# Kernel optimization log

Hardware: AMD Instinct MI355X
Metric: run time of the kernel (lower is better)

The kernel has to match this reference:

```python
import jax, jax.numpy as jnp
import numpy as np

HIDDEN = 512
HEAD = 64
SEQ = 2048
CHUNK = 256
GAMMA = 0.96875
SCALE_BASE = 512.0


def _xpos(x, downscale):
    # x: [B, L, hd]; XPOS with offset=0 (scale rows == length, no trimming needed)
    B, L, hd = x.shape
    half = hd // 2
    scale_vec = (jnp.arange(0, hd, 2, dtype=jnp.float32) + 0.4 * hd) / (1.4 * hd)  # [half]
    power = jnp.arange(L, dtype=jnp.float32) / SCALE_BASE                          # [L]
    scale = scale_vec[None, :] ** power[:, None]                                   # [L, half]
    inv_freq = 1.0 / (10000.0 ** (jnp.arange(half, dtype=jnp.float32) / half))
    sinusoid = jnp.arange(L, dtype=jnp.float32)[:, None] * inv_freq[None, :]       # [L, half]
    sin, cos = jnp.sin(sinusoid), jnp.cos(sinusoid)
    if downscale:
        scale = 1.0 / scale
    # duplicate_interleave: repeat each column twice -> [L, hd]
    sin_f = jnp.repeat(sin * scale, 2, axis=-1)
    cos_f = jnp.repeat(cos * scale, 2, axis=-1)
    x1 = x[:, :, 0::2]
    x2 = x[:, :, 1::2]
    rot = jnp.stack((-x2, x1), axis=-1).reshape(B, L, hd)  # rotate_every_two
    return x * cos_f + rot * sin_f


def _D_parallel():
    # D[i, j] = gamma^|i-j| if j < (i//chunk + 1)*chunk else 0 (block-causal with in-chunk lookahead)
    i = jnp.arange(SEQ)[:, None]
    j = jnp.arange(SEQ)[None, :]
    j_max = (i // CHUNK + 1) * CHUNK
    decay = GAMMA ** jnp.abs(i - j).astype(jnp.float32)
    return jnp.where(j < j_max, decay, 0.0)  # gamma>0 so no NaNs to scrub


def setup_inputs() -> dict:
    key = jax.random.key(0)
    k1, k2, k3, k4 = jax.random.split(key, 4)
    X = jax.random.normal(k1, (8, SEQ, HIDDEN), dtype=jnp.float32)
    W_Q = jax.random.normal(k2, (HIDDEN, HEAD), dtype=jnp.float32) / HIDDEN
    W_K = jax.random.normal(k3, (HIDDEN, HEAD), dtype=jnp.float32) / HIDDEN
    W_V = jax.random.normal(k4, (HIDDEN, HEAD), dtype=jnp.float32) / HIDDEN
    return {"X": X, "W_Q": W_Q, "W_K": W_K, "W_V": W_V}


def reference(X, W_Q, W_K, W_V):
    Q = _xpos(X @ W_Q, downscale=False)   # [B, S, H]
    K = _xpos(X @ W_K, downscale=True)    # [B, S, H]
    V = X @ W_V                           # [B, S, V]
    D = _D_parallel()                     # [S, S]
    scores = jnp.einsum('bqh,bkh->bqk', Q, K) * D[None]
    return jnp.einsum('bqk,bkv->bqv', scores, V)
```

## Files before the change

kernel.cpp:

```cpp
#include <hip/hip_runtime.h>
#include <hip/hip_bf16.h>


typedef __attribute__((ext_vector_type(8))) short short8;
typedef __attribute__((ext_vector_type(4))) float floatx4;

#define LOG2GAMMA (-0.04580350f)
#define GINV      (1.0f / 0.96875f)

static __device__ __forceinline__ unsigned short f2bf(float f) {
    __hip_bfloat16 h = __float2bfloat16(f);
    return *reinterpret_cast<unsigned short*>(&h);
}


__global__ __launch_bounds__(256) void prep_kernel(
    const float* __restrict__ Wq, const float* __restrict__ Wk,
    const float* __restrict__ Wv,
    __hip_bfloat16* __restrict__ Wfrag, float* __restrict__ tabs)
{
    int idx = blockIdx.x * 256 + threadIdx.x;
    const int WF_N = 192 * 512;
    if (idx < WF_N) {
        int j    = idx & 7;
        int n15  = (idx >> 3) & 15;
        int quad = (idx >> 7) & 3;
        int kkg  = (idx >> 9) & 15;
        int tile = idx >> 13;
        int n = tile * 16 + n15;
        int k = kkg * 32 + quad * 8 + j;
        int m = n >> 6, c = n & 63;
        const float* W = (m == 0) ? Wq : ((m == 1) ? Wk : Wv);
        Wfrag[idx] = __float2bfloat16(W[k * 64 + c]);
    } else {
        int t2 = idx - WF_N;
        if (t2 < 4 * 2048 * 32) {
            int tab = t2 >> 16;
            int rem = t2 & 65535;
            int pos = rem >> 5;
            int t   = rem & 31;
            float inv_freq = powf(10000.0f, -(float)t / 32.0f);
            float sinus = (float)pos * inv_freq;
            float s = sinf(sinus), c = cosf(sinus);
            float sv = (2.0f * (float)t + 0.4f * 64.0f) / (1.4f * 64.0f);
            float power = (float)pos / 512.0f;
            float scl = powf(sv, (tab >= 2) ? -power : power);
            tabs[t2] = ((tab & 1) == 0) ? c * scl : s * scl;
        }
    }
}

__global__ __launch_bounds__(256, 4) void proj_kernel(
    const float* __restrict__ X, const __hip_bfloat16* __restrict__ Wfrag,
    const float* __restrict__ tabs,
    __hip_bfloat16* __restrict__ Qfrag, __hip_bfloat16* __restrict__ Kfrag,
    __hip_bfloat16* __restrict__ Vfrag, __hip_bfloat16* __restrict__ Ktfrag)
{
    __shared__ __hip_bfloat16 smem[32 * 520];

    int tid = threadIdx.x;
    int r0 = blockIdx.x * 32;
    int nh = tid >> 6, lane = tid & 63, quad = lane >> 4, l15 = lane & 15;

#pragma unroll
    for (int u = 0; u < 16; u++) {
        int f = u * 256 + tid;
        int row = f >> 7, c = f & 127;
        float4 v = *(const float4*)(X + (r0 + row) * 512 + c * 4);
        ushort4 pk;
        pk.x = f2bf(v.x); pk.y = f2bf(v.y); pk.z = f2bf(v.z); pk.w = f2bf(v.w);
        *(ushort4*)&smem[row * 520 + c * 4] = pk;
    }
    __syncthreads();

    floatx4 acc[6];
#pragma unroll
    for (int t = 0; t < 6; t++) acc[t] = (floatx4){0.f, 0.f, 0.f, 0.f};

#pragma unroll
    for (int ks = 0; ks < 16; ks++) {
        short8 a0 = *(const short8*)&smem[l15 * 520 + ks * 32 + quad * 8];
        short8 a1 = *(const short8*)&smem[(16 + l15) * 520 + ks * 32 + quad * 8];
#pragma unroll
        for (int tl = 0; tl < 3; tl++) {
            int tile = nh * 3 + tl;
            short8 bfr = *(const short8*)(Wfrag + ((tile * 16 + ks) * 64 + lane) * 8);
            acc[tl * 2 + 0] = __builtin_amdgcn_mfma_f32_16x16x32_bf16(a0, bfr, acc[tl * 2 + 0], 0, 0, 0);
            acc[tl * 2 + 1] = __builtin_amdgcn_mfma_f32_16x16x32_bf16(a1, bfr, acc[tl * 2 + 1], 0, 0, 0);
        }
    }
    __syncthreads();

    __hip_bfloat16* bufQ = smem;
    __hip_bfloat16* bufK = smem + 2304;
    __hip_bfloat16* bufV = smem + 4608;
    int b = r0 >> 11, n0 = r0 & 2047;

#pragma unroll
    for (int tl = 0; tl < 3; tl++) {
        int t = nh * 3 + tl;
#pragma unroll
        for (int r = 0; r < 2; r++) {
#pragma unroll
            for (int rg = 0; rg < 4; rg++) {
                int row = r * 16 + quad * 4 + rg;
                int n = n0 + row;
                float val = acc[tl * 2 + r][rg];
                float prt = __shfl_xor(val, 1, 64);
                if (t < 4) {
                    int ch = t * 16 + l15, tt = ch >> 1;
                    float co = tabs[n * 32 + tt];
                    float si = tabs[65536 + n * 32 + tt];
                    float o = (l15 & 1) ? (val * co + prt * si) : (val * co - prt * si);
                    bufQ[row * 72 + ch] = __float2bfloat16(o);
                } else if (t < 8) {
                    int ch = (t - 4) * 16 + l15, tt = ch >> 1;
                    float co = tabs[131072 + n * 32 + tt];
                    float si = tabs[196608 + n * 32 + tt];
                    float o = (l15 & 1) ? (val * co + prt * si) : (val * co - prt * si);
                    bufK[row * 72 + ch] = __float2bfloat16(o);
                } else {
                    int ch = (t - 8) * 16 + l15;
                    bufV[ch * 40 + row] = __float2bfloat16(val);
                }
            }
        }
    }
    __syncthreads();

    {
        int tile2 = tid >> 7, kk = (tid >> 6) & 1, ln = tid & 63;
        int q2 = ln >> 4, m15 = ln & 15;
        size_t qkbase = ((((size_t)b * 128 + (n0 >> 4) + tile2) * 2 + kk) * 64 + ln) * 8;
        uint4 vq = *(const uint4*)&bufQ[(tile2 * 16 + m15) * 72 + kk * 32 + q2 * 8];
        *(uint4*)(Qfrag + qkbase) = vq;
        uint4 vk = *(const uint4*)&bufK[(tile2 * 16 + m15) * 72 + kk * 32 + q2 * 8];
        *(uint4*)(Kfrag + qkbase) = vk;
        int t2 = tid >> 6;
        uint4 vv = *(const uint4*)&bufV[(t2 * 16 + m15) * 40 + q2 * 8];
        *(uint4*)(Vfrag + ((((size_t)b * 64 + (n0 >> 5)) * 4 + t2) * 64 + ln) * 8) = vv;
    }
    {
        int wdt = tid >> 6, ln2 = tid & 63;
        int q2 = ln2 >> 4, m15 = ln2 & 15;
        int jb0 = (n0 & 255) + q2 * 8;
        float sc = exp2f(LOG2GAMMA * (float)(255 - jb0));
        short8 pk;
#pragma unroll
        for (int jj = 0; jj < 8; jj++) {
            float v = __bfloat162float(bufK[(q2 * 8 + jj) * 72 + wdt * 16 + m15]) * sc;
            pk[jj] = (short)f2bf(v);
            sc *= GINV;
        }
        int c = n0 >> 8, ksg = (n0 >> 5) & 7;
        *(short8*)(Ktfrag + ((((size_t)(b * 8 + c) * 4 + wdt) * 8 + ksg) * 64 + ln2) * 8) = pk;
    }
}

__global__ __launch_bounds__(256, 2) void zk_kernel(
    const __hip_bfloat16* __restrict__ Ktfrag,
    const __hip_bfloat16* __restrict__ Vfrag, float* __restrict__ Zf)
{
    __shared__ float zz[64 * 68];

    int tid = threadIdx.x;
    int b = blockIdx.x >> 4, c = (blockIdx.x >> 1) & 7, kh = blockIdx.x & 1;
    int w = tid >> 6, lane = tid & 63, quad = lane >> 4, l15 = lane & 15;

    floatx4 acc[4];
#pragma unroll
    for (int t = 0; t < 4; t++) acc[t] = (floatx4){0.f, 0.f, 0.f, 0.f};

#pragma unroll
    for (int ks = 0; ks < 4; ks++) {
        int ksg = kh * 4 + ks;
        short8 a = *(const short8*)(Ktfrag +
            ((((size_t)(b * 8 + c) * 4 + w) * 8 + ksg) * 64 + lane) * 8);
#pragma unroll
        for (int vt = 0; vt < 4; vt++) {
            short8 bfr = *(const short8*)(Vfrag +
                ((((size_t)b * 64 + c * 8 + ksg) * 4 + vt) * 64 + lane) * 8);
            acc[vt] = __builtin_amdgcn_mfma_f32_16x16x32_bf16(a, bfr, acc[vt], 0, 0, 0);
        }
    }
#pragma unroll
    for (int vt = 0; vt < 4; vt++)
#pragma unroll
        for (int rg = 0; rg < 4; rg++)
            zz[(w * 16 + quad * 4 + rg) * 68 + vt * 16 + l15] = acc[vt][rg];
    __syncthreads();

    {
        int vt = tid >> 6;
#pragma unroll
        for (int kk = 0; kk < 2; kk++) {
            float v[8];
#pragma unroll
            for (int jd = 0; jd < 8; jd++)
                v[jd] = zz[(kk * 32 + quad * 8 + jd) * 68 + vt * 16 + l15];
            float* zp = Zf +
                ((((((size_t)(b * 8 + c) * 2 + kh) * 4 + vt) * 2 + kk) * 64 + lane) * 8);
            *(float4*)zp       = (float4){v[0], v[1], v[2], v[3]};
            *(float4*)(zp + 4) = (float4){v[4], v[5], v[6], v[7]};
        }
    }
}

__global__ __launch_bounds__(128, 4) void attn_kernel(
    const __hip_bfloat16* __restrict__ Qfrag, const __hip_bfloat16* __restrict__ Kfrag,
    const __hip_bfloat16* __restrict__ Vfrag, const float* __restrict__ Zf,
    float* __restrict__ out)
{
    __shared__ __hip_bfloat16 P[2 * 16 * 132];
    __shared__ float obuf[16 * 68];

    int tid = threadIdx.x;
    int b = blockIdx.x >> 7, qt = blockIdx.x & 127;
    int qc = qt >> 4;
    int h = tid >> 6, lane = tid & 63, quad = lane >> 4, l15 = lane & 15;
    __hip_bfloat16* Pw = P + h * 2112;

    short8 qf[2];
#pragma unroll
    for (int kk = 0; kk < 2; kk++)
        qf[kk] = *(const short8*)(Qfrag + (((size_t)(b * 128 + qt) * 2 + kk) * 64 + lane) * 8);

    floatx4 o[4];
#pragma unroll
    for (int t = 0; t < 4; t++) o[t] = (floatx4){0.f, 0.f, 0.f, 0.f};

    int il0 = (qt & 15) * 16 + quad * 4;

#pragma unroll
    for (int g = 0; g < 2; g++) {
        floatx4 s[4];
#pragma unroll
        for (int t = 0; t < 4; t++) s[t] = (floatx4){0.f, 0.f, 0.f, 0.f};
#pragma unroll
        for (int t = 0; t < 4; t++) {
            int kt = qc * 16 + h * 8 + g * 4 + t;
#pragma unroll
            for (int kk = 0; kk < 2; kk++) {
                short8 bfr = *(const short8*)(Kfrag +
                    (((size_t)(b * 128 + kt) * 2 + kk) * 64 + lane) * 8);
                s[t] = __builtin_amdgcn_mfma_f32_16x16x32_bf16(qf[kk], bfr, s[t], 0, 0, 0);
            }
        }
#pragma unroll
        for (int t = 0; t < 4; t++) {
            int jl = h * 128 + (g * 4 + t) * 16 + l15;
#pragma unroll
            for (int rg = 0; rg < 4; rg++) {
                int d = il0 + rg - jl; d = (d < 0) ? -d : d;
                float p = s[t][rg] * exp2f(LOG2GAMMA * (float)d);
                Pw[(quad * 4 + rg) * 132 + (g * 4 + t) * 16 + l15] = __float2bfloat16(p);
            }
        }
    }
#pragma unroll
    for (int ks = 0; ks < 4; ks++) {
        short8 a = *(const short8*)&Pw[l15 * 132 + ks * 32 + quad * 8];
#pragma unroll
        for (int vt = 0; vt < 4; vt++) {
            short8 bfr = *(const short8*)(Vfrag +
                ((((size_t)b * 64 + qc * 8 + h * 4 + ks) * 4 + vt) * 64 + lane) * 8);
            o[vt] = __builtin_amdgcn_mfma_f32_16x16x32_bf16(a, bfr, o[vt], 0, 0, 0);
        }
    }

    if (qc > 0) {
        floatx4 oc[4];
#pragma unroll
        for (int t = 0; t < 4; t++) oc[t] = (floatx4){0.f, 0.f, 0.f, 0.f};
        int nz = (qc < 3) ? qc : 3;
        float cm1 = exp2f(LOG2GAMMA * 256.0f);
        float cm2 = exp2f(LOG2GAMMA * 512.0f);
#pragma unroll
        for (int vt = 0; vt < 4; vt++) {
            float hv[8];
#pragma unroll
            for (int jd = 0; jd < 8; jd++) hv[jd] = 0.f;
            for (int m = 0; m < nz; m++) {
                float cm = (m == 0) ? 1.0f : ((m == 1) ? cm1 : cm2);
#pragma unroll
                for (int kh = 0; kh < 2; kh++) {
                    const float* zp = Zf +
                        ((((((size_t)(b * 8 + qc - 1 - m) * 2 + kh) * 4 + vt) * 2 + h) * 64 + lane) * 8);
                    float4 z0 = *(const float4*)zp;
                    float4 z1 = *(const float4*)(zp + 4);
                    hv[0] += cm * z0.x; hv[1] += cm * z0.y;
                    hv[2] += cm * z0.z; hv[3] += cm * z0.w;
                    hv[4] += cm * z1.x; hv[5] += cm * z1.y;
                    hv[6] += cm * z1.z; hv[7] += cm * z1.w;
                }
            }
            short8 hb;
#pragma unroll
            for (int jd = 0; jd < 8; jd++) hb[jd] = (short)f2bf(hv[jd]);
            oc[vt] = __builtin_amdgcn_mfma_f32_16x16x32_bf16(qf[h], hb, oc[vt], 0, 0, 0);
        }
        float rs[4];
#pragma unroll
        for (int rg = 0; rg < 4; rg++)
            rs[rg] = exp2f(LOG2GAMMA * (float)(il0 + rg + 1));
#pragma unroll
        for (int vt = 0; vt < 4; vt++)
#pragma unroll
            for (int rg = 0; rg < 4; rg++)
                o[vt][rg] += oc[vt][rg] * rs[rg];
    }

    if (h == 1) {
#pragma unroll
        for (int vt = 0; vt < 4; vt++)
#pragma unroll
            for (int rg = 0; rg < 4; rg++)
                obuf[(quad * 4 + rg) * 68 + vt * 16 + l15] = o[vt][rg];
    }
    __syncthreads();
    if (h == 0) {
        int rbase = b * 2048 + qt * 16 + quad * 4;
#pragma unroll
        for (int vt = 0; vt < 4; vt++)
#pragma unroll
            for (int rg = 0; rg < 4; rg++)
                out[(size_t)(rbase + rg) * 64 + vt * 16 + l15] =
                    o[vt][rg] + obuf[(quad * 4 + rg) * 68 + vt * 16 + l15];
    }
}

extern "C" void kernel_launch(void* const* d_in, const int* in_sizes, int n_in,
                              void* d_out, int out_size, void* d_ws, size_t ws_size,
                              hipStream_t stream) {
    const float* X  = (const float*)d_in[0];
    const float* Wq = (const float*)d_in[1];
    const float* Wk = (const float*)d_in[2];
    const float* Wv = (const float*)d_in[3];
    float* out = (float*)d_out;

    char* ws = (char*)d_ws;
    __hip_bfloat16* Wfrag  = (__hip_bfloat16*)(ws);
    float*          tabs   = (float*)(ws + 196608);
    __hip_bfloat16* Qfrag  = (__hip_bfloat16*)(ws + 1245184);
    __hip_bfloat16* Kfrag  = (__hip_bfloat16*)(ws + 3342336);
    __hip_bfloat16* Vfrag  = (__hip_bfloat16*)(ws + 5439488);
    __hip_bfloat16* Ktfrag = (__hip_bfloat16*)(ws + 7536640);
    float*          Zf     = (float*)(ws + 9633792);

    prep_kernel<<<1408, 256, 0, stream>>>(Wq, Wk, Wv, Wfrag, tabs);
    proj_kernel<<<512, 256, 0, stream>>>(X, Wfrag, tabs, Qfrag, Kfrag, Vfrag, Ktfrag);
    zk_kernel<<<128, 256, 0, stream>>>(Ktfrag, Vfrag, Zf);
    attn_kernel<<<1024, 128, 0, stream>>>(Qfrag, Kfrag, Vfrag, Zf, out);
}
```

Baseline: 111.5 us.

## Load X fragments directly from global into MFMA registers, use fast math in prep

The projection kernel no longer stages the 32x512 X tile through shared memory. Each wave reads its own fp32 fragments from global memory, converts them to bf16 in registers, and feeds the MFMAs directly. This drops the staging copy and a barrier and shrinks LDS use, which may raise occupancy. The cost is that all four waves now read the same X rows (4x redundant global/L2 traffic) with less coalesced 32-byte accesses. The prep kernel also replaces powf/sinf/cosf with exp2f/__log2f/__sinf/__cosf, trading table accuracy for speed, which may hurt precision at large angles.

```diff
diff --git a/kernel.cpp b/kernel.cpp
--- a/kernel.cpp
+++ b/kernel.cpp
@@ -7,6 +7,7 @@
 
 #define LOG2GAMMA (-0.04580350f)
 #define GINV      (1.0f / 0.96875f)
+#define LOG2_10K  (13.287712379549449f)
 
 static __device__ __forceinline__ unsigned short f2bf(float f) {
     __hip_bfloat16 h = __float2bfloat16(f);
@@ -39,12 +40,13 @@
             int rem = t2 & 65535;
             int pos = rem >> 5;
             int t   = rem & 31;
-            float inv_freq = powf(10000.0f, -(float)t / 32.0f);
+            float inv_freq = exp2f((float)t * (-LOG2_10K / 32.0f));
             float sinus = (float)pos * inv_freq;
-            float s = sinf(sinus), c = cosf(sinus);
-            float sv = (2.0f * (float)t + 0.4f * 64.0f) / (1.4f * 64.0f);
-            float power = (float)pos / 512.0f;
-            float scl = powf(sv, (tab >= 2) ? -power : power);
+            float s = __sinf(sinus), c = __cosf(sinus);
+            float sv = (2.0f * (float)t + 25.6f) / 89.6f;
+            float power = (float)pos * (1.0f / 512.0f);
+            float e = ((tab >= 2) ? -power : power) * __log2f(sv);
+            float scl = exp2f(e);
             tabs[t2] = ((tab & 1) == 0) ? c * scl : s * scl;
         }
     }
@@ -56,22 +58,14 @@
     __hip_bfloat16* __restrict__ Qfrag, __hip_bfloat16* __restrict__ Kfrag,
     __hip_bfloat16* __restrict__ Vfrag, __hip_bfloat16* __restrict__ Ktfrag)
 {
-    __shared__ __hip_bfloat16 smem[32 * 520];
+    __shared__ __hip_bfloat16 smem[7168];
 
     int tid = threadIdx.x;
     int r0 = blockIdx.x * 32;
     int nh = tid >> 6, lane = tid & 63, quad = lane >> 4, l15 = lane & 15;
 
-#pragma unroll
-    for (int u = 0; u < 16; u++) {
-        int f = u * 256 + tid;
-        int row = f >> 7, c = f & 127;
-        float4 v = *(const float4*)(X + (r0 + row) * 512 + c * 4);
-        ushort4 pk;
-        pk.x = f2bf(v.x); pk.y = f2bf(v.y); pk.z = f2bf(v.z); pk.w = f2bf(v.w);
-        *(ushort4*)&smem[row * 520 + c * 4] = pk;
-    }
-    __syncthreads();
+    const float* xp0 = X + (size_t)(r0 + l15) * 512 + quad * 8;
+    const float* xp1 = xp0 + 16 * 512;
 
     floatx4 acc[6];
 #pragma unroll
@@ -79,8 +73,19 @@
 
 #pragma unroll
     for (int ks = 0; ks < 16; ks++) {
-        short8 a0 = *(const short8*)&smem[l15 * 520 + ks * 32 + quad * 8];
-        short8 a1 = *(const short8*)&smem[(16 + l15) * 520 + ks * 32 + quad * 8];
+        float4 x00 = *(const float4*)(xp0 + ks * 32);
+        float4 x01 = *(const float4*)(xp0 + ks * 32 + 4);
+        float4 x10 = *(const float4*)(xp1 + ks * 32);
+        float4 x11 = *(const float4*)(xp1 + ks * 32 + 4);
+        short8 a0, a1;
+        a0[0] = (short)f2bf(x00.x); a0[1] = (short)f2bf(x00.y);
+        a0[2] = (short)f2bf(x00.z); a0[3] = (short)f2bf(x00.w);
+        a0[4] = (short)f2bf(x01.x); a0[5] = (short)f2bf(x01.y);
+        a0[6] = (short)f2bf(x01.z); a0[7] = (short)f2bf(x01.w);
+        a1[0] = (short)f2bf(x10.x); a1[1] = (short)f2bf(x10.y);
+        a1[2] = (short)f2bf(x10.z); a1[3] = (short)f2bf(x10.w);
+        a1[4] = (short)f2bf(x11.x); a1[5] = (short)f2bf(x11.y);
+        a1[6] = (short)f2bf(x11.z); a1[7] = (short)f2bf(x11.w);
 #pragma unroll
         for (int tl = 0; tl < 3; tl++) {
             int tile = nh * 3 + tl;
@@ -89,7 +94,6 @@
             acc[tl * 2 + 1] = __builtin_amdgcn_mfma_f32_16x16x32_bf16(a1, bfr, acc[tl * 2 + 1], 0, 0, 0);
         }
     }
-    __syncthreads();
 
     __hip_bfloat16* bufQ = smem;
     __hip_bfloat16* bufK = smem + 2304;
```

New measurement: 116.4 us. 1.04x slower.
